# Kernel tuning notes

Hardware: AMD Instinct MI355X
Metric: run time of the kernel (lower is better)

## Reference

```python
import jax, jax.numpy as jnp
import numpy as np


def setup_inputs() -> dict:
    key = jax.random.key(0)
    ks = jax.random.split(key, 7)
    B, T, D, H = 32, 2048, 512, 512
    s = 1.0 / np.sqrt(H)
    return {
        "input": jax.random.normal(ks[0], (B, T, D), dtype=jnp.float32),
        "h0": jax.random.normal(ks[1], (B, H), dtype=jnp.float32),
        "c0": jax.random.normal(ks[2], (B, H), dtype=jnp.float32),
        "W_ih": jax.random.normal(ks[3], (4 * H, D), dtype=jnp.float32) * s,
        "W_hh": jax.random.normal(ks[4], (4 * H, H), dtype=jnp.float32) * s,
        "b_ih": jax.random.normal(ks[5], (4 * H,), dtype=jnp.float32) * s,
        "b_hh": jax.random.normal(ks[6], (4 * H,), dtype=jnp.float32) * s,
    }


def _lstm(input, h0, c0, W_ih, W_hh, b_ih, b_hh):
    H = h0.shape[-1]
    # Precompute input projections for all timesteps: [T, B, 4H]
    x_proj = jnp.einsum('btd,gd->tbg', input, W_ih) + b_ih + b_hh

    def step(carry, xp):
        h, c = carry
        gates = xp + h @ W_hh.T  # [B, 4H]
        i, f, g, o = jnp.split(gates, 4, axis=-1)  # PyTorch gate order
        i = jax.nn.sigmoid(i)
        f = jax.nn.sigmoid(f)
        g = jnp.tanh(g)
        o = jax.nn.sigmoid(o)
        c_new = f * c + i * g
        h_new = o * jnp.tanh(c_new)
        return (h_new, c_new), None

    (h, c), _ = jax.lax.scan(step, (h0, c0), x_proj)
    return h, c


def reference(input, h0, c0, W_ih, W_hh, b_ih, b_hh):
    return _lstm(input, h0, c0, W_ih, W_hh, b_ih, b_hh)
```

## Files before the change

### kernel.cpp

```cpp
#include <hip/hip_runtime.h>

#define B_ 32
#define T_ 2048
#define D_ 512
#define H_ 512
#define G4 2048
#define NREC 64
#define NWRK 192

typedef short short8 __attribute__((ext_vector_type(8)));
typedef float floatv16 __attribute__((ext_vector_type(16)));
typedef float floatv4 __attribute__((ext_vector_type(4)));

static __device__ __forceinline__ unsigned short f2bf(float f) {
  union { float f; unsigned u; } v; v.f = f;
  unsigned u = v.u;
  u += 0x7fffu + ((u >> 16) & 1u);
  return (unsigned short)(u >> 16);
}
static __device__ __forceinline__ float bf2f(unsigned short h) {
  union { unsigned u; float f; } v; v.u = ((unsigned)h) << 16;
  return v.f;
}
static __device__ __forceinline__ float sigm(float x) { return 1.0f / (1.0f + __expf(-x)); }
static __device__ __forceinline__ float tanh_(float x) {
  float e = __expf(-2.0f * fabsf(x));
  float t = (1.0f - e) / (1.0f + e);
  return copysignf(t, x);
}

#define MFMA32(A, Bv, C) __builtin_amdgcn_mfma_f32_32x32x16_bf16((A), (Bv), (C), 0, 0, 0)

__global__ __launch_bounds__(256) void cvt_kernel(
    const float* __restrict__ Wih, const float* __restrict__ Whh,
    const float* __restrict__ bih, const float* __restrict__ bhh,
    const float* __restrict__ h0, const float* __restrict__ c0,
    short* __restrict__ wih_hi, short* __restrict__ wih_lo, short* __restrict__ whh_hi,
    float* __restrict__ bias, short* __restrict__ hbuf0, float* __restrict__ cws) {
  int i = blockIdx.x * 256 + threadIdx.x;
  if (i < G4 * D_) {
    float w = Wih[i];
    unsigned short hi = f2bf(w);
    wih_hi[i] = (short)hi;
    wih_lo[i] = (short)f2bf(w - bf2f(hi));
    whh_hi[i] = (short)f2bf(Whh[i]);
  }
  if (i < G4) bias[i] = bih[i] + bhh[i];
  if (i < B_ * H_) { hbuf0[i] = (short)f2bf(h0[i]); cws[i] = c0[i]; }
}

__global__ __launch_bounds__(256, 1) void xproj_kernel(
    const float* __restrict__ input,
    const short* __restrict__ wih_hi, const short* __restrict__ wih_lo,
    const float* __restrict__ bias, float* __restrict__ xp, int t0, int TC) {
  __shared__ short xlo_lds[4 * 8192];
  const int tid = threadIdx.x;
  const int wv = tid >> 6, l = tid & 63;
  const int wid = blockIdx.x * 4 + wv;
  const int lt = wid >> 3, nb = wid & 7;
  const int t = t0 + lt;
  const int lb = l & 31, hb = l >> 5;
  const float* xrow = input + ((size_t)lb * T_ + t) * D_ + hb * 8;
  short* slo = xlo_lds + wv * 8192;
  short8 xhi[32];
#pragma unroll
  for (int kb = 0; kb < 32; ++kb) {
    floatv4 x0 = *(const floatv4*)(xrow + kb * 16);
    floatv4 x1 = *(const floatv4*)(xrow + kb * 16 + 4);
    float xs[8] = {x0[0], x0[1], x0[2], x0[3], x1[0], x1[1], x1[2], x1[3]};
    short8 hi, lo;
#pragma unroll
    for (int j = 0; j < 8; ++j) {
      unsigned short h = f2bf(xs[j]);
      hi[j] = (short)h;
      lo[j] = (short)f2bf(xs[j] - bf2f(h));
    }
    xhi[kb] = hi;
    *(short8*)(slo + (kb * 64 + l) * 8) = lo;
  }
  for (int nt = 0; nt < 8; ++nt) {
    const int n0 = nb * 256 + nt * 32;
    const short* whbase = wih_hi + (size_t)(n0 + lb) * D_ + hb * 8;
    const short* wlbase = wih_lo + (size_t)(n0 + lb) * D_ + hb * 8;
    floatv16 a0, a1;
#pragma unroll
    for (int i = 0; i < 16; ++i) { a0[i] = 0.0f; a1[i] = 0.0f; }
#pragma unroll
    for (int kb = 0; kb < 32; ++kb) {
      short8 whi = *(const short8*)(whbase + kb * 16);
      short8 wlo = *(const short8*)(wlbase + kb * 16);
      short8 xl = *(const short8*)(slo + (kb * 64 + l) * 8);
      a0 = MFMA32(whi, xhi[kb], a0);
      a1 = MFMA32(whi, xl, a1);
      a1 = MFMA32(wlo, xhi[kb], a1);
    }
#pragma unroll
    for (int r = 0; r < 16; ++r) {
      int row = (r & 3) + 8 * (r >> 2) + 4 * hb;
      int n = n0 + row;
      xp[((size_t)lt * G4 + n) * B_ + lb] = a0[r] + a1[r] + bias[n];
    }
  }
}

__global__ __launch_bounds__(64, 1) void fused_step(
    const float* __restrict__ input,
    const short* __restrict__ wih_hi, const short* __restrict__ wih_lo,
    const float* __restrict__ bias, const short* __restrict__ whh,
    short* __restrict__ hbuf, float* __restrict__ cws, int* __restrict__ flags,
    const float* __restrict__ xpc, float* __restrict__ xpn,
    float* __restrict__ out, int t0, int TC, int writeOut, int doNext) {
  __shared__ short slo[16384];
  const int l = threadIdx.x;
  const int lb = l & 31, hb = l >> 5;

  if (blockIdx.x < NREC) {
    const int w = blockIdx.x;
    const int ngl = (lb >> 3) * H_ + w * 8 + (lb & 7);
    short8 Wf[32];
#pragma unroll
    for (int kb = 0; kb < 32; ++kb)
      Wf[kb] = *(const short8*)(whh + (size_t)ngl * H_ + kb * 16 + hb * 8);
    float c4[4], h4[4];
#pragma unroll
    for (int q = 0; q < 4; ++q) c4[q] = cws[lb * H_ + w * 8 + 4 * hb + q];

    for (int t = t0; t < t0 + TC; ++t) {
      const float* xpt = xpc + (size_t)(t - t0) * G4 * B_;
      float xpv[16];
#pragma unroll
      for (int g = 0; g < 4; ++g)
#pragma unroll
        for (int q = 0; q < 4; ++q)
          xpv[g * 4 + q] = xpt[(size_t)(g * H_ + w * 8 + 4 * hb + q) * B_ + lb];

      if (t > 0) {
        int v;
        do {
          v = __hip_atomic_load(flags + l * 16, __ATOMIC_ACQUIRE, __HIP_MEMORY_SCOPE_AGENT);
        } while (!__all(v >= t));
      }

      const short* hsrc = hbuf + (t & 1) * (B_ * H_) + lb * H_ + hb * 8;
      floatv16 D0, D1;
#pragma unroll
      for (int i = 0; i < 16; ++i) { D0[i] = 0.0f; D1[i] = 0.0f; }
#pragma unroll
      for (int kb = 0; kb < 32; kb += 2) {
        short8 hf0 = *(const short8*)(hsrc + kb * 16);
        short8 hf1 = *(const short8*)(hsrc + kb * 16 + 16);
        D0 = MFMA32(Wf[kb], hf0, D0);
        D1 = MFMA32(Wf[kb + 1], hf1, D1);
      }

      union { unsigned short s[4]; unsigned long long u; } pk;
#pragma unroll
      for (int q = 0; q < 4; ++q) {
        float gi = D0[q] + D1[q] + xpv[q];
        float gf = D0[4 + q] + D1[4 + q] + xpv[4 + q];
        float gg = D0[8 + q] + D1[8 + q] + xpv[8 + q];
        float go = D0[12 + q] + D1[12 + q] + xpv[12 + q];
        float iv = sigm(gi), fv = sigm(gf), gv = tanh_(gg), ov = sigm(go);
        c4[q] = fv * c4[q] + iv * gv;
        h4[q] = ov * tanh_(c4[q]);
        pk.s[q] = f2bf(h4[q]);
      }
      unsigned long long* hdst = (unsigned long long*)(hbuf + ((t + 1) & 1) * (B_ * H_) +
                                                       lb * H_ + w * 8 + 4 * hb);
      __hip_atomic_store(hdst, pk.u, __ATOMIC_RELAXED, __HIP_MEMORY_SCOPE_AGENT);
      if (l == 0)
        __hip_atomic_store(flags + w * 16, t + 1, __ATOMIC_RELEASE, __HIP_MEMORY_SCOPE_AGENT);
    }

#pragma unroll
    for (int q = 0; q < 4; ++q) cws[lb * H_ + w * 8 + 4 * hb + q] = c4[q];
    if (writeOut) {
#pragma unroll
      for (int q = 0; q < 4; ++q) {
        out[lb * H_ + w * 8 + 4 * hb + q] = h4[q];
        out[B_ * H_ + lb * H_ + w * 8 + 4 * hb + q] = c4[q];
      }
    }
  } else if (doNext) {
    const int wkr = blockIdx.x - NREC;
    const int t0n = t0 + TC;
    for (int j = wkr; j < TC * 8; j += NWRK) {
      const int lt = j >> 3, nb = j & 7;
      const int t = t0n + lt;
      const float* xrow = input + ((size_t)lb * T_ + t) * D_ + hb * 8;
      short8 xhi[32];
#pragma unroll
      for (int kb = 0; kb < 32; ++kb) {
        floatv4 x0 = *(const floatv4*)(xrow + kb * 16);
        floatv4 x1 = *(const floatv4*)(xrow + kb * 16 + 4);
        float xs[8] = {x0[0], x0[1], x0[2], x0[3], x1[0], x1[1], x1[2], x1[3]};
        short8 hi, lo;
#pragma unroll
        for (int jj = 0; jj < 8; ++jj) {
          unsigned short h = f2bf(xs[jj]);
          hi[jj] = (short)h;
          lo[jj] = (short)f2bf(xs[jj] - bf2f(h));
        }
        xhi[kb] = hi;
        *(short8*)(slo + (kb * 64 + l) * 8) = lo;
      }
      for (int nt = 0; nt < 8; ++nt) {
        const int n0 = nb * 256 + nt * 32;
        const short* whbase = wih_hi + (size_t)(n0 + lb) * D_ + hb * 8;
        const short* wlbase = wih_lo + (size_t)(n0 + lb) * D_ + hb * 8;
        floatv16 a0, a1;
#pragma unroll
        for (int i = 0; i < 16; ++i) { a0[i] = 0.0f; a1[i] = 0.0f; }
#pragma unroll
        for (int kb = 0; kb < 32; ++kb) {
          short8 whi = *(const short8*)(whbase + kb * 16);
          short8 wlo = *(const short8*)(wlbase + kb * 16);
          short8 xl = *(const short8*)(slo + (kb * 64 + l) * 8);
          a0 = MFMA32(whi, xhi[kb], a0);
          a1 = MFMA32(whi, xl, a1);
          a1 = MFMA32(wlo, xhi[kb], a1);
        }
#pragma unroll
        for (int r = 0; r < 16; ++r) {
          int row = (r & 3) + 8 * (r >> 2) + 4 * hb;
          int n = n0 + row;
          xpn[((size_t)lt * G4 + n) * B_ + lb] = a0[r] + a1[r] + bias[n];
        }
      }
    }
  }
}

extern "C" void kernel_launch(void* const* d_in, const int* in_sizes, int n_in,
                              void* d_out, int out_size, void* d_ws, size_t ws_size,
                              hipStream_t stream) {
  (void)in_sizes; (void)n_in; (void)out_size;
  const float* input = (const float*)d_in[0];
  const float* h0 = (const float*)d_in[1];
  const float* c0 = (const float*)d_in[2];
  const float* Wih = (const float*)d_in[3];
  const float* Whh = (const float*)d_in[4];
  const float* bih = (const float*)d_in[5];
  const float* bhh = (const float*)d_in[6];

  char* ws = (char*)d_ws;
  short* wih_hi = (short*)(ws);
  short* wih_lo = (short*)(ws + (2ull << 20));
  short* whh_hi = (short*)(ws + (4ull << 20));
  float* bias = (float*)(ws + (6ull << 20));
  short* hbuf = (short*)(ws + (6ull << 20) + 65536);
  float* cws = (float*)(ws + (6ull << 20) + 131072);
  int* flags = (int*)(ws + (6ull << 20) + 196608);

  int TC = 32;
  while (TC < 256 && (8ull << 20) + (size_t)(TC * 2) * (G4 * B_ * 4) <= ws_size) TC <<= 1;
  const int nch = T_ / TC;
  float* xpA = (float*)(ws + (8ull << 20));
  float* xpB = xpA + (size_t)TC * G4 * B_;

  hipMemsetAsync(flags, 0, 4096, stream);
  cvt_kernel<<<dim3((G4 * D_ + 255) / 256), dim3(256), 0, stream>>>(
      Wih, Whh, bih, bhh, h0, c0, wih_hi, wih_lo, whh_hi, bias, hbuf, cws);
  xproj_kernel<<<dim3(TC * 2), dim3(256), 0, stream>>>(input, wih_hi, wih_lo, bias,
                                                       xpA, 0, TC);
  for (int k = 0; k < nch; ++k) {
    float* cur = (k & 1) ? xpB : xpA;
    float* nxt = (k & 1) ? xpA : xpB;
    fused_step<<<dim3(NREC + NWRK), dim3(64), 0, stream>>>(
        input, wih_hi, wih_lo, bias, whh_hi, hbuf, cws, flags, cur, nxt,
        (float*)d_out, k * TC, TC, (k == nch - 1) ? 1 : 0, (k < nch - 1) ? 1 : 0);
  }
}
```

Before: 12.69 ms.

## Halve recurrent workgroups, each computing sixteen hidden units per step

Reduces the number of recurrent blocks from 64 to 32, so each block holds two W_hh fragments in registers and issues twice the MFMAs per timestep. Fewer participants in the per-step flag barrier should cut spin-wait and synchronization latency on the serial critical path. In exchange, each block does more compute per step and needs far more registers (64 short8 weight fragments plus four accumulators), which risks spilling.

```diff
diff --git a/kernel.cpp b/kernel.cpp
--- a/kernel.cpp
+++ b/kernel.cpp
@@ -5,7 +5,7 @@
 #define D_ 512
 #define H_ 512
 #define G4 2048
-#define NREC 64
+#define NREC 32
 #define NWRK 192
 
 typedef short short8 __attribute__((ext_vector_type(8)));
@@ -116,69 +116,89 @@
 
   if (blockIdx.x < NREC) {
     const int w = blockIdx.x;
-    const int ngl = (lb >> 3) * H_ + w * 8 + (lb & 7);
-    short8 Wf[32];
-#pragma unroll
-    for (int kb = 0; kb < 32; ++kb)
-      Wf[kb] = *(const short8*)(whh + (size_t)ngl * H_ + kb * 16 + hb * 8);
-    float c4[4], h4[4];
-#pragma unroll
-    for (int q = 0; q < 4; ++q) c4[q] = cws[lb * H_ + w * 8 + 4 * hb + q];
+    const int ngl0 = (lb >> 3) * H_ + w * 16 + (lb & 7);
+    const int ngl1 = ngl0 + 8;
+    short8 Wf0[32], Wf1[32];
+#pragma unroll
+    for (int kb = 0; kb < 32; ++kb) {
+      Wf0[kb] = *(const short8*)(whh + (size_t)ngl0 * H_ + kb * 16 + hb * 8);
+      Wf1[kb] = *(const short8*)(whh + (size_t)ngl1 * H_ + kb * 16 + hb * 8);
+    }
+    float c8[8], h8[8];
+#pragma unroll
+    for (int q = 0; q < 8; ++q)
+      c8[q] = cws[lb * H_ + w * 16 + (q >> 2) * 8 + 4 * hb + (q & 3)];
 
     for (int t = t0; t < t0 + TC; ++t) {
       const float* xpt = xpc + (size_t)(t - t0) * G4 * B_;
-      float xpv[16];
+      float xpv[32];
 #pragma unroll
       for (int g = 0; g < 4; ++g)
 #pragma unroll
-        for (int q = 0; q < 4; ++q)
-          xpv[g * 4 + q] = xpt[(size_t)(g * H_ + w * 8 + 4 * hb + q) * B_ + lb];
+        for (int q = 0; q < 8; ++q)
+          xpv[g * 8 + q] =
+              xpt[(size_t)(g * H_ + w * 16 + (q >> 2) * 8 + 4 * hb + (q & 3)) * B_ + lb];
 
       if (t > 0) {
         int v;
         do {
-          v = __hip_atomic_load(flags + l * 16, __ATOMIC_ACQUIRE, __HIP_MEMORY_SCOPE_AGENT);
+          v = __hip_atomic_load(flags + (l & 31) * 16, __ATOMIC_ACQUIRE,
+                                __HIP_MEMORY_SCOPE_AGENT);
         } while (!__all(v >= t));
       }
 
       const short* hsrc = hbuf + (t & 1) * (B_ * H_) + lb * H_ + hb * 8;
-      floatv16 D0, D1;
-#pragma unroll
-      for (int i = 0; i < 16; ++i) { D0[i] = 0.0f; D1[i] = 0.0f; }
+      floatv16 D0a, D1a, D0b, D1b;
+#pragma unroll
+      for (int i = 0; i < 16; ++i) { D0a[i] = 0.0f; D1a[i] = 0.0f; D0b[i] = 0.0f; D1b[i] = 0.0f; }
 #pragma unroll
       for (int kb = 0; kb < 32; kb += 2) {
         short8 hf0 = *(const short8*)(hsrc + kb * 16);
         short8 hf1 = *(const short8*)(hsrc + kb * 16 + 16);
-        D0 = MFMA32(Wf[kb], hf0, D0);
-        D1 = MFMA32(Wf[kb + 1], hf1, D1);
-      }
-
-      union { unsigned short s[4]; unsigned long long u; } pk;
+        D0a = MFMA32(Wf0[kb], hf0, D0a);
+        D1a = MFMA32(Wf0[kb + 1], hf1, D1a);
+        D0b = MFMA32(Wf1[kb], hf0, D0b);
+        D1b = MFMA32(Wf1[kb + 1], hf1, D1b);
+      }
+
+      union { unsigned short s[4]; unsigned long long u; } pk0, pk1;
 #pragma unroll
       for (int q = 0; q < 4; ++q) {
-        float gi = D0[q] + D1[q] + xpv[q];
-        float gf = D0[4 + q] + D1[4 + q] + xpv[4 + q];
-        float gg = D0[8 + q] + D1[8 + q] + xpv[8 + q];
-        float go = D0[12 + q] + D1[12 + q] + xpv[12 + q];
+        float gi = D0a[q] + D1a[q] + xpv[q];
+        float gf = D0a[4 + q] + D1a[4 + q] + xpv[8 + q];
+        float gg = D0a[8 + q] + D1a[8 + q] + xpv[16 + q];
+        float go = D0a[12 + q] + D1a[12 + q] + xpv[24 + q];
         float iv = sigm(gi), fv = sigm(gf), gv = tanh_(gg), ov = sigm(go);
-        c4[q] = fv * c4[q] + iv * gv;
-        h4[q] = ov * tanh_(c4[q]);
-        pk.s[q] = f2bf(h4[q]);
-      }
-      unsigned long long* hdst = (unsigned long long*)(hbuf + ((t + 1) & 1) * (B_ * H_) +
-                                                       lb * H_ + w * 8 + 4 * hb);
-      __hip_atomic_store(hdst, pk.u, __ATOMIC_RELAXED, __HIP_MEMORY_SCOPE_AGENT);
+        c8[q] = fv * c8[q] + iv * gv;
+        h8[q] = ov * tanh_(c8[q]);
+        pk0.s[q] = f2bf(h8[q]);
+        float gi1 = D0b[q] + D1b[q] + xpv[4 + q];
+        float gf1 = D0b[4 + q] + D1b[4 + q] + xpv[12 + q];
+        float gg1 = D0b[8 + q] + D1b[8 + q] + xpv[20 + q];
+        float go1 = D0b[12 + q] + D1b[12 + q] + xpv[28 + q];
+        float iv1 = sigm(gi1), fv1 = sigm(gf1), gv1 = tanh_(gg1), ov1 = sigm(go1);
+        c8[4 + q] = fv1 * c8[4 + q] + iv1 * gv1;
+        h8[4 + q] = ov1 * tanh_(c8[4 + q]);
+        pk1.s[q] = f2bf(h8[4 + q]);
+      }
+      short* hdb = hbuf + ((t + 1) & 1) * (B_ * H_) + lb * H_ + w * 16 + 4 * hb;
+      __hip_atomic_store((unsigned long long*)hdb, pk0.u, __ATOMIC_RELAXED,
+                         __HIP_MEMORY_SCOPE_AGENT);
+      __hip_atomic_store((unsigned long long*)(hdb + 8), pk1.u, __ATOMIC_RELAXED,
+                         __HIP_MEMORY_SCOPE_AGENT);
       if (l == 0)
         __hip_atomic_store(flags + w * 16, t + 1, __ATOMIC_RELEASE, __HIP_MEMORY_SCOPE_AGENT);
     }
 
 #pragma unroll
-    for (int q = 0; q < 4; ++q) cws[lb * H_ + w * 8 + 4 * hb + q] = c4[q];
+    for (int q = 0; q < 8; ++q)
+      cws[lb * H_ + w * 16 + (q >> 2) * 8 + 4 * hb + (q & 3)] = c8[q];
     if (writeOut) {
 #pragma unroll
-      for (int q = 0; q < 4; ++q) {
-        out[lb * H_ + w * 8 + 4 * hb + q] = h4[q];
-        out[B_ * H_ + lb * H_ + w * 8 + 4 * hb + q] = c4[q];
+      for (int q = 0; q < 8; ++q) {
+        int u = w * 16 + (q >> 2) * 8 + 4 * hb + (q & 3);
+        out[lb * H_ + u] = h8[q];
+        out[B_ * H_ + lb * H_ + u] = c8[q];
       }
     }
   } else if (doNext) {
```

After: 14.91 ms. 1.17x slower.
